# Kernel tuning notes

Hardware: AMD Instinct MI355X
Metric: run time of the kernel (lower is better)

Reference implementation:

```python
import jax, jax.numpy as jnp
from jax import lax
import numpy as np

CLIP = 20.0  # DeepSpeech clipped-ReLU bound


def setup_inputs() -> dict:
    key = jax.random.key(0)
    k1, k2, k3 = jax.random.split(key, 3)
    B, T, F, U_ = 32, 800, 161, 1024
    inputs = jax.random.normal(k1, (B, T, F), dtype=jnp.float32)
    W = jax.random.normal(k2, (F, U_), dtype=jnp.float32) * 0.05
    U = jax.random.normal(k3, (U_, U_), dtype=jnp.float32) * 0.02
    b = jnp.zeros((U_,), dtype=jnp.float32)
    return {"inputs": inputs, "W": W, "U": U, "b": b}


def reference(inputs, W, U, b):
    # inputs: [B, T, F]; shared cell weights for both directions.
    B = inputs.shape[0]
    units = U.shape[0]
    # Precompute input projection for all timesteps: [T, B, units]
    xW = (jnp.einsum('btf,fu->btu', inputs, W) + b).transpose(1, 0, 2)
    h0 = jnp.zeros((B, units), dtype=inputs.dtype)

    def step(h, x):
        h = jnp.minimum(jax.nn.relu(x + h @ U), CLIP)
        return h, None

    hf, _ = lax.scan(step, h0, xW)                 # final state, forward direction
    hb, _ = lax.scan(step, h0, xW, reverse=True)   # final state, go_backwards
    return hf + hb
```

## Files before the change

kernel.cpp:

```cpp
#include <hip/hip_runtime.h>
#include <hip/hip_bf16.h>

#define T_STEPS 800
#define BATCH   32
#define FEAT    161
#define UNITS   1024
#define CLIPV   20.0f

typedef __attribute__((ext_vector_type(8))) short short8;
typedef __attribute__((ext_vector_type(4))) float f32x4;
typedef unsigned short u16;
typedef unsigned int   u32;
typedef unsigned long long u64;

__device__ __forceinline__ float bf16_f(u16 u) {
    return __uint_as_float(((u32)u) << 16);
}
__device__ __forceinline__ u16 bf16_rn(float x) {
    __hip_bfloat16 b = __float2bfloat16(x);
    return *(u16*)&b;
}
__device__ __forceinline__ u64 ld_agent_u64(const u64* p) {
    return __hip_atomic_load(p, __ATOMIC_RELAXED, __HIP_MEMORY_SCOPE_AGENT);
}
__device__ __forceinline__ float ld_agent_f(const float* p) {
    return __hip_atomic_load(p, __ATOMIC_RELAXED, __HIP_MEMORY_SCOPE_AGENT);
}
__device__ __forceinline__ void st_agent_f(float* p, float v) {
    __hip_atomic_store(p, v, __ATOMIC_RELAXED, __HIP_MEMORY_SCOPE_AGENT);
}
__device__ __forceinline__ void st_agent_u32(u32* p, u32 v) {
    __hip_atomic_store(p, v, __ATOMIC_RELAXED, __HIP_MEMORY_SCOPE_AGENT);
}
__device__ __forceinline__ short8 ld_agent_b16x8(const u16* p) {
    union { u64 q[2]; short8 v; } u;
    u.q[0] = ld_agent_u64((const u64*)p);
    u.q[1] = ld_agent_u64((const u64*)p + 1);
    return u.v;
}

__global__ __launch_bounds__(256) void init_ws(float* hbuf, u32* flags) {
    int gid = blockIdx.x * 256 + threadIdx.x;
    for (int i = gid; i < 2 * 64 * UNITS; i += 64 * 256) hbuf[i] = 0.f;
    if (gid < 256) flags[gid] = 0u;
}

__global__ __launch_bounds__(256) void u_split_t(const float* __restrict__ U,
                                                 u16* __restrict__ Ut1,
                                                 u16* __restrict__ Ut2,
                                                 u16* __restrict__ Ut3) {
    __shared__ float tile[32][33];
    int bx = blockIdx.x, by = blockIdx.y;
    int lx = threadIdx.x & 31;
    int ly4 = (threadIdx.x >> 5) * 4;
    #pragma unroll
    for (int j = 0; j < 4; ++j)
        tile[ly4 + j][lx] = U[(size_t)(by * 32 + ly4 + j) * UNITS + bx * 32 + lx];
    __syncthreads();
    #pragma unroll
    for (int j = 0; j < 4; ++j) {
        float x = tile[lx][ly4 + j];
        size_t o = (size_t)(bx * 32 + ly4 + j) * UNITS + by * 32 + lx;
        u16 s1 = bf16_rn(x);  float r1 = x - bf16_f(s1);
        u16 s2 = bf16_rn(r1); float r2 = r1 - bf16_f(s2);
        u16 s3 = bf16_rn(r2);
        Ut1[o] = s1; Ut2[o] = s2; Ut3[o] = s3;
    }
}

__global__ __launch_bounds__(256) void xw_gemm(const float* __restrict__ inp,
                                               const float* __restrict__ W,
                                               const float* __restrict__ bias,
                                               float* __restrict__ xW) {
    __shared__ float xs[8 * FEAT];
    int t = blockIdx.x;
    int b0 = blockIdx.y * 8;
    int tid = threadIdx.x;

    for (int i = tid; i < 8 * FEAT; i += 256) {
        int j = i / FEAT;
        int f = i - j * FEAT;
        xs[i] = inp[((size_t)(b0 + j) * T_STEPS + t) * FEAT + f];
    }
    __syncthreads();

    float bv[4];
    #pragma unroll
    for (int c = 0; c < 4; ++c) bv[c] = bias[tid + c * 256];

    float acc[8][4];
    #pragma unroll
    for (int j = 0; j < 8; ++j)
        #pragma unroll
        for (int c = 0; c < 4; ++c) acc[j][c] = bv[c];

    for (int f = 0; f < FEAT; ++f) {
        float w0 = W[(size_t)f * UNITS + tid];
        float w1 = W[(size_t)f * UNITS + tid + 256];
        float w2 = W[(size_t)f * UNITS + tid + 512];
        float w3 = W[(size_t)f * UNITS + tid + 768];
        #pragma unroll
        for (int j = 0; j < 8; ++j) {
            float xv = xs[j * FEAT + f];
            acc[j][0] += xv * w0;
            acc[j][1] += xv * w1;
            acc[j][2] += xv * w2;
            acc[j][3] += xv * w3;
        }
    }

    #pragma unroll
    for (int j = 0; j < 8; ++j)
        #pragma unroll
        for (int c = 0; c < 4; ++c)
            xW[((size_t)t * BATCH + b0 + j) * UNITS + tid + c * 256] = acc[j][c];
}

__global__ __launch_bounds__(512) void rnn_scan(
        const float* __restrict__ xW,
        const u16* __restrict__ Ut1, const u16* __restrict__ Ut2,
        const u16* __restrict__ Ut3,
        float* __restrict__ hbuf, u32* __restrict__ flags,
        float* __restrict__ out) {
    __shared__ f32x4 red[14][64];

    const int tid  = threadIdx.x;
    const int bk   = blockIdx.x;
    const int lane = tid & 63;
    const int kq   = tid >> 6;
    const int quad = lane >> 4;
    const int n16  = lane & 15;
    const int rg   = bk & 3;
    const int ug   = bk >> 2;
    const int R0   = rg * 16;
    const int u0   = ug * 32;
    const int dir  = rg >> 1;

    short8 bfr[4][2][3];
    #pragma unroll
    for (int ks = 0; ks < 4; ++ks) {
        const int koff = kq * 128 + ks * 32 + quad * 8;
        #pragma unroll
        for (int nq = 0; nq < 2; ++nq) {
            const size_t ub = (size_t)(u0 + nq * 16 + n16) * UNITS + koff;
            bfr[ks][nq][0] = ld_agent_b16x8(Ut1 + ub);
            bfr[ks][nq][1] = ld_agent_b16x8(Ut2 + ub);
            bfr[ks][nq][2] = ld_agent_b16x8(Ut3 + ub);
        }
    }

    const size_t HS = (size_t)64 * UNITS;
    u32* myflag = flags + rg * 32 + ug;
    const u64* srcflag = (const u64*)(flags + rg * 32 + kq * 4);

    for (int t = 0; t < T_STEPS; ++t) {
        const size_t sb = (size_t)(t & 1) * HS;
        const size_t db = sb ^ HS;

        float xp[2][4];
        if (kq == 0) {
            const int xt = dir ? (T_STEPS - 1 - t) : t;
            #pragma unroll
            for (int nq = 0; nq < 2; ++nq)
                #pragma unroll
                for (int j = 0; j < 4; ++j) {
                    const int b = (R0 + quad * 4 + j) & 31;
                    xp[nq][j] = xW[(size_t)xt * (BATCH * UNITS) +
                                   (size_t)b * UNITS + u0 + nq * 16 + n16];
                }
        }

        const u32 tgt = (u32)t;
        for (;;) {
            u64 qa = ld_agent_u64(srcflag);
            u64 qb = ld_agent_u64(srcflag + 1);
            u32 f0 = (u32)qa, f1 = (u32)(qa >> 32);
            u32 f2 = (u32)qb, f3 = (u32)(qb >> 32);
            if (f0 >= tgt && f1 >= tgt && f2 >= tgt && f3 >= tgt) break;
        }

        f32x4 acc[2][2] = {{{0.f,0.f,0.f,0.f},{0.f,0.f,0.f,0.f}},
                           {{0.f,0.f,0.f,0.f},{0.f,0.f,0.f,0.f}}};
        #pragma unroll
        for (int ks = 0; ks < 4; ++ks) {
            const float* ap = hbuf + sb + (size_t)(R0 + n16) * UNITS +
                              kq * 128 + ks * 32 + quad * 8;
            union { u64 q[4]; float f[8]; u32 u[8]; } hv;
            hv.q[0] = ld_agent_u64((const u64*)ap);
            hv.q[1] = ld_agent_u64((const u64*)ap + 1);
            hv.q[2] = ld_agent_u64((const u64*)ap + 2);
            hv.q[3] = ld_agent_u64((const u64*)ap + 3);
            short8 a1, a2, a3;
            #pragma unroll
            for (int j = 0; j < 8; ++j) {
                float x = hv.f[j];
                u16 s1 = (u16)(hv.u[j] >> 16);
                float r1 = x - bf16_f(s1);
                u16 s2 = (u16)(__float_as_uint(r1) >> 16);
                float r2 = r1 - bf16_f(s2);
                u16 s3 = (u16)(__float_as_uint(r2) >> 16);
                a1[j] = (short)s1; a2[j] = (short)s2; a3[j] = (short)s3;
            }
            #pragma unroll
            for (int nq = 0; nq < 2; ++nq) {
                acc[nq][0] = __builtin_amdgcn_mfma_f32_16x16x32_bf16(a1, bfr[ks][nq][0], acc[nq][0], 0, 0, 0);
                acc[nq][1] = __builtin_amdgcn_mfma_f32_16x16x32_bf16(a2, bfr[ks][nq][0], acc[nq][1], 0, 0, 0);
                acc[nq][0] = __builtin_amdgcn_mfma_f32_16x16x32_bf16(a1, bfr[ks][nq][1], acc[nq][0], 0, 0, 0);
                acc[nq][1] = __builtin_amdgcn_mfma_f32_16x16x32_bf16(a2, bfr[ks][nq][1], acc[nq][1], 0, 0, 0);
                acc[nq][0] = __builtin_amdgcn_mfma_f32_16x16x32_bf16(a1, bfr[ks][nq][2], acc[nq][0], 0, 0, 0);
                acc[nq][1] = __builtin_amdgcn_mfma_f32_16x16x32_bf16(a3, bfr[ks][nq][0], acc[nq][1], 0, 0, 0);
            }
        }
        f32x4 c0 = acc[0][0] + acc[0][1];
        f32x4 c1 = acc[1][0] + acc[1][1];

        if (kq) {
            red[(kq - 1) * 2 + 0][lane] = c0;
            red[(kq - 1) * 2 + 1][lane] = c1;
        }
        __syncthreads();
        if (kq == 0) {
            #pragma unroll
            for (int w = 0; w < 7; ++w) {
                c0 += red[w * 2 + 0][lane];
                c1 += red[w * 2 + 1][lane];
            }
            float* hdst = hbuf + db;
            #pragma unroll
            for (int nq = 0; nq < 2; ++nq)
                #pragma unroll
                for (int j = 0; j < 4; ++j) {
                    float a = (nq ? c1[j] : c0[j]) + xp[nq][j];
                    a = fminf(fmaxf(a, 0.f), CLIPV);
                    st_agent_f(hdst + (size_t)(R0 + quad * 4 + j) * UNITS +
                               u0 + nq * 16 + n16, a);
                }
        }
        __syncthreads();
        if (tid == 0) st_agent_u32(myflag, (u32)(t + 1));
    }

    if (rg < 2) {
        const u32* bwd = flags + (rg + 2) * 32 + ug;
        while (__hip_atomic_load(bwd, __ATOMIC_RELAXED,
                                 __HIP_MEMORY_SCOPE_AGENT) < (u32)T_STEPS) {}
        const int r = tid >> 5, c = tid & 31;
        const int b = R0 + r;
        float hf = ld_agent_f(hbuf + (size_t)b * UNITS + u0 + c);
        float hb = ld_agent_f(hbuf + (size_t)(b + 32) * UNITS + u0 + c);
        out[(size_t)b * UNITS + u0 + c] = hf + hb;
    }
}

extern "C" void kernel_launch(void* const* d_in, const int* in_sizes, int n_in,
                              void* d_out, int out_size, void* d_ws, size_t ws_size,
                              hipStream_t stream) {
    const float* inp  = (const float*)d_in[0];
    const float* W    = (const float*)d_in[1];
    const float* U    = (const float*)d_in[2];
    const float* bias = (const float*)d_in[3];
    float* out = (float*)d_out;

    u16*   Ut1 = (u16*)d_ws;
    u16*   Ut2 = Ut1 + (size_t)UNITS * UNITS;
    u16*   Ut3 = Ut2 + (size_t)UNITS * UNITS;
    float* xW  = (float*)(Ut3 + (size_t)UNITS * UNITS);
    float* hbuf = xW + (size_t)T_STEPS * BATCH * UNITS;
    u32*   flags = (u32*)(hbuf + (size_t)2 * 64 * UNITS);

    init_ws<<<64, 256, 0, stream>>>(hbuf, flags);
    u_split_t<<<dim3(32, 32), 256, 0, stream>>>(U, Ut1, Ut2, Ut3);
    xw_gemm<<<dim3(800, 4), 256, 0, stream>>>(inp, W, bias, xW);

    void* args[] = {(void*)&xW, (void*)&Ut1, (void*)&Ut2, (void*)&Ut3,
                    (void*)&hbuf, (void*)&flags, (void*)&out};
    hipLaunchCooperativeKernel((const void*)rnn_scan, dim3(128), dim3(512),
                               args, 0, stream);
}
```

Before: 4.332 ms.

## Replace per-block step flags with tagged hidden-state words for inter-block sync

Each hidden-state element is now stored as a 64-bit word that packs the float value with its timestep tag. Consumers spin directly on the data they need, so the separate flag store and the flag poll round-trip go away. The cross-wave reduction and epilogue are also spread over all 512 threads instead of one wave doing the add, clip and store. The cost is doubled hidden-state traffic, 8-byte loads per element, and polling on data words that may contend with producers' stores.

```diff
diff --git a/kernel.cpp b/kernel.cpp
--- a/kernel.cpp
+++ b/kernel.cpp
@@ -23,26 +23,19 @@
 __device__ __forceinline__ u64 ld_agent_u64(const u64* p) {
     return __hip_atomic_load(p, __ATOMIC_RELAXED, __HIP_MEMORY_SCOPE_AGENT);
 }
-__device__ __forceinline__ float ld_agent_f(const float* p) {
-    return __hip_atomic_load(p, __ATOMIC_RELAXED, __HIP_MEMORY_SCOPE_AGENT);
-}
-__device__ __forceinline__ void st_agent_f(float* p, float v) {
+__device__ __forceinline__ void st_agent_u64(u64* p, u64 v) {
     __hip_atomic_store(p, v, __ATOMIC_RELAXED, __HIP_MEMORY_SCOPE_AGENT);
 }
-__device__ __forceinline__ void st_agent_u32(u32* p, u32 v) {
-    __hip_atomic_store(p, v, __ATOMIC_RELAXED, __HIP_MEMORY_SCOPE_AGENT);
-}
-__device__ __forceinline__ short8 ld_agent_b16x8(const u16* p) {
+__device__ __forceinline__ short8 ld_b16x8(const u16* p) {
     union { u64 q[2]; short8 v; } u;
     u.q[0] = ld_agent_u64((const u64*)p);
     u.q[1] = ld_agent_u64((const u64*)p + 1);
     return u.v;
 }
 
-__global__ __launch_bounds__(256) void init_ws(float* hbuf, u32* flags) {
+__global__ __launch_bounds__(256) void init_ws(u64* htag) {
     int gid = blockIdx.x * 256 + threadIdx.x;
-    for (int i = gid; i < 2 * 64 * UNITS; i += 64 * 256) hbuf[i] = 0.f;
-    if (gid < 256) flags[gid] = 0u;
+    for (int i = gid; i < 2 * 64 * UNITS; i += 64 * 256) htag[i] = 0ull;
 }
 
 __global__ __launch_bounds__(256) void u_split_t(const float* __restrict__ U,
@@ -120,9 +113,8 @@
         const float* __restrict__ xW,
         const u16* __restrict__ Ut1, const u16* __restrict__ Ut2,
         const u16* __restrict__ Ut3,
-        float* __restrict__ hbuf, u32* __restrict__ flags,
-        float* __restrict__ out) {
-    __shared__ f32x4 red[14][64];
+        u64* __restrict__ htag, float* __restrict__ out) {
+    __shared__ f32x4 red[16][64];
 
     const int tid  = threadIdx.x;
     const int bk   = blockIdx.x;
@@ -136,6 +128,14 @@
     const int u0   = ug * 32;
     const int dir  = rg >> 1;
 
+    const int erow = tid >> 5;
+    const int ecol = tid & 31;
+    const int enq  = ecol >> 4;
+    const int el16 = (erow >> 2) * 16 + (ecol & 15);
+    const int ereg = erow & 3;
+    const int eb   = (R0 + erow) & 31;
+    const size_t edst = (size_t)(R0 + erow) * UNITS + u0 + ecol;
+
     short8 bfr[4][2][3];
     #pragma unroll
     for (int ks = 0; ks < 4; ++ks) {
@@ -143,58 +143,44 @@
         #pragma unroll
         for (int nq = 0; nq < 2; ++nq) {
             const size_t ub = (size_t)(u0 + nq * 16 + n16) * UNITS + koff;
-            bfr[ks][nq][0] = ld_agent_b16x8(Ut1 + ub);
-            bfr[ks][nq][1] = ld_agent_b16x8(Ut2 + ub);
-            bfr[ks][nq][2] = ld_agent_b16x8(Ut3 + ub);
+            bfr[ks][nq][0] = ld_b16x8(Ut1 + ub);
+            bfr[ks][nq][1] = ld_b16x8(Ut2 + ub);
+            bfr[ks][nq][2] = ld_b16x8(Ut3 + ub);
         }
     }
 
     const size_t HS = (size_t)64 * UNITS;
-    u32* myflag = flags + rg * 32 + ug;
-    const u64* srcflag = (const u64*)(flags + rg * 32 + kq * 4);
 
     for (int t = 0; t < T_STEPS; ++t) {
         const size_t sb = (size_t)(t & 1) * HS;
         const size_t db = sb ^ HS;
-
-        float xp[2][4];
-        if (kq == 0) {
-            const int xt = dir ? (T_STEPS - 1 - t) : t;
-            #pragma unroll
-            for (int nq = 0; nq < 2; ++nq)
-                #pragma unroll
-                for (int j = 0; j < 4; ++j) {
-                    const int b = (R0 + quad * 4 + j) & 31;
-                    xp[nq][j] = xW[(size_t)xt * (BATCH * UNITS) +
-                                   (size_t)b * UNITS + u0 + nq * 16 + n16];
-                }
-        }
-
-        const u32 tgt = (u32)t;
-        for (;;) {
-            u64 qa = ld_agent_u64(srcflag);
-            u64 qb = ld_agent_u64(srcflag + 1);
-            u32 f0 = (u32)qa, f1 = (u32)(qa >> 32);
-            u32 f2 = (u32)qb, f3 = (u32)(qb >> 32);
-            if (f0 >= tgt && f1 >= tgt && f2 >= tgt && f3 >= tgt) break;
-        }
+        const u32 tagv = (u32)t;
+
+        const int xt = dir ? (T_STEPS - 1 - t) : t;
+        const float xwv = xW[(size_t)xt * (BATCH * UNITS) +
+                             (size_t)eb * UNITS + u0 + ecol];
 
         f32x4 acc[2][2] = {{{0.f,0.f,0.f,0.f},{0.f,0.f,0.f,0.f}},
                            {{0.f,0.f,0.f,0.f},{0.f,0.f,0.f,0.f}}};
         #pragma unroll
         for (int ks = 0; ks < 4; ++ks) {
-            const float* ap = hbuf + sb + (size_t)(R0 + n16) * UNITS +
-                              kq * 128 + ks * 32 + quad * 8;
-            union { u64 q[4]; float f[8]; u32 u[8]; } hv;
-            hv.q[0] = ld_agent_u64((const u64*)ap);
-            hv.q[1] = ld_agent_u64((const u64*)ap + 1);
-            hv.q[2] = ld_agent_u64((const u64*)ap + 2);
-            hv.q[3] = ld_agent_u64((const u64*)ap + 3);
+            const u64* src = htag + sb + (size_t)(R0 + n16) * UNITS +
+                             kq * 128 + ks * 32 + quad * 8;
+            u64 p[8];
+            for (;;) {
+                #pragma unroll
+                for (int j = 0; j < 8; ++j) p[j] = ld_agent_u64(src + j);
+                bool ok = true;
+                #pragma unroll
+                for (int j = 0; j < 8; ++j) ok &= ((u32)(p[j] >> 32) == tagv);
+                if (__all(ok)) break;
+            }
             short8 a1, a2, a3;
             #pragma unroll
             for (int j = 0; j < 8; ++j) {
-                float x = hv.f[j];
-                u16 s1 = (u16)(hv.u[j] >> 16);
+                u32 xb = (u32)p[j];
+                float x = __uint_as_float(xb);
+                u16 s1 = (u16)(xb >> 16);
                 float r1 = x - bf16_f(s1);
                 u16 s2 = (u16)(__float_as_uint(r1) >> 16);
                 float r2 = r1 - bf16_f(s2);
@@ -211,44 +197,28 @@
                 acc[nq][1] = __builtin_amdgcn_mfma_f32_16x16x32_bf16(a3, bfr[ks][nq][0], acc[nq][1], 0, 0, 0);
             }
         }
-        f32x4 c0 = acc[0][0] + acc[0][1];
-        f32x4 c1 = acc[1][0] + acc[1][1];
-
-        if (kq) {
-            red[(kq - 1) * 2 + 0][lane] = c0;
-            red[(kq - 1) * 2 + 1][lane] = c1;
-        }
+
+        red[kq * 2 + 0][lane] = acc[0][0] + acc[0][1];
+        red[kq * 2 + 1][lane] = acc[1][0] + acc[1][1];
         __syncthreads();
-        if (kq == 0) {
-            #pragma unroll
-            for (int w = 0; w < 7; ++w) {
-                c0 += red[w * 2 + 0][lane];
-                c1 += red[w * 2 + 1][lane];
-            }
-            float* hdst = hbuf + db;
-            #pragma unroll
-            for (int nq = 0; nq < 2; ++nq)
-                #pragma unroll
-                for (int j = 0; j < 4; ++j) {
-                    float a = (nq ? c1[j] : c0[j]) + xp[nq][j];
-                    a = fminf(fmaxf(a, 0.f), CLIPV);
-                    st_agent_f(hdst + (size_t)(R0 + quad * 4 + j) * UNITS +
-                               u0 + nq * 16 + n16, a);
-                }
-        }
+
+        float s = 0.f;
+        #pragma unroll
+        for (int w = 0; w < 8; ++w) s += red[w * 2 + enq][el16][ereg];
+        float a = fminf(fmaxf(s + xwv, 0.f), CLIPV);
+        st_agent_u64(htag + db + edst,
+                     ((u64)(u32)(t + 1) << 32) | (u64)__float_as_uint(a));
         __syncthreads();
-        if (tid == 0) st_agent_u32(myflag, (u32)(t + 1));
     }
 
     if (rg < 2) {
-        const u32* bwd = flags + (rg + 2) * 32 + ug;
-        while (__hip_atomic_load(bwd, __ATOMIC_RELAXED,
-                                 __HIP_MEMORY_SCOPE_AGENT) < (u32)T_STEPS) {}
-        const int r = tid >> 5, c = tid & 31;
-        const int b = R0 + r;
-        float hf = ld_agent_f(hbuf + (size_t)b * UNITS + u0 + c);
-        float hb = ld_agent_f(hbuf + (size_t)(b + 32) * UNITS + u0 + c);
-        out[(size_t)b * UNITS + u0 + c] = hf + hb;
+        const u64* pf = htag + (size_t)(R0 + erow) * UNITS + u0 + ecol;
+        const u64* pb = htag + (size_t)(R0 + erow + 32) * UNITS + u0 + ecol;
+        u64 vf, vb;
+        while ((u32)((vf = ld_agent_u64(pf)) >> 32) != (u32)T_STEPS) {}
+        while ((u32)((vb = ld_agent_u64(pb)) >> 32) != (u32)T_STEPS) {}
+        out[(size_t)(R0 + erow) * UNITS + u0 + ecol] =
+            __uint_as_float((u32)vf) + __uint_as_float((u32)vb);
     }
 }
 
@@ -265,15 +235,14 @@
     u16*   Ut2 = Ut1 + (size_t)UNITS * UNITS;
     u16*   Ut3 = Ut2 + (size_t)UNITS * UNITS;
     float* xW  = (float*)(Ut3 + (size_t)UNITS * UNITS);
-    float* hbuf = xW + (size_t)T_STEPS * BATCH * UNITS;
-    u32*   flags = (u32*)(hbuf + (size_t)2 * 64 * UNITS);
-
-    init_ws<<<64, 256, 0, stream>>>(hbuf, flags);
+    u64*   htag = (u64*)(xW + (size_t)T_STEPS * BATCH * UNITS);
+
+    init_ws<<<64, 256, 0, stream>>>(htag);
     u_split_t<<<dim3(32, 32), 256, 0, stream>>>(U, Ut1, Ut2, Ut3);
     xw_gemm<<<dim3(800, 4), 256, 0, stream>>>(inp, W, bias, xW);
 
     void* args[] = {(void*)&xW, (void*)&Ut1, (void*)&Ut2, (void*)&Ut3,
-                    (void*)&hbuf, (void*)&flags, (void*)&out};
+                    (void*)&htag, (void*)&out};
     hipLaunchCooperativeKernel((const void*)rnn_scan, dim3(128), dim3(512),
                                args, 0, stream);
 }
```

New measurement: 7.198 ms. 1.66x slower.

## Pin each row group to one XCD and sync via XCD-local L2 with fallback

Applied to the files above, without the earlier changes.

Launches 256 blocks and keeps only those whose block index maps to XCD groups 0-3, so each batch-row group's 32 blocks are intended to share one XCD. Hidden-state and flag traffic then uses plain stores and sc0 loads that stay in the local L2, avoiding the agent-scope coherence path. A runtime XCD-ID check picks the mode. A poll timeout demotes a group to the agent-scope protocol if the placement assumption fails. The final states are copied to a separate buffer and combined across groups after a global counter. This adds inline-asm memory ordering that is hard to verify and depends on how the hardware assigns blocks to XCDs.

```diff
diff --git a/kernel.cpp b/kernel.cpp
--- a/kernel.cpp
+++ b/kernel.cpp
@@ -6,9 +6,11 @@
 #define FEAT    161
 #define UNITS   1024
 #define CLIPV   20.0f
+#define POLL_TIMEOUT 4096
 
 typedef __attribute__((ext_vector_type(8))) short short8;
 typedef __attribute__((ext_vector_type(4))) float f32x4;
+typedef __attribute__((ext_vector_type(4))) unsigned int u32x4;
 typedef unsigned short u16;
 typedef unsigned int   u32;
 typedef unsigned long long u64;
@@ -23,13 +25,16 @@
 __device__ __forceinline__ u64 ld_agent_u64(const u64* p) {
     return __hip_atomic_load(p, __ATOMIC_RELAXED, __HIP_MEMORY_SCOPE_AGENT);
 }
+__device__ __forceinline__ u32 ld_agent_u32(const u32* p) {
+    return __hip_atomic_load(p, __ATOMIC_RELAXED, __HIP_MEMORY_SCOPE_AGENT);
+}
 __device__ __forceinline__ float ld_agent_f(const float* p) {
     return __hip_atomic_load(p, __ATOMIC_RELAXED, __HIP_MEMORY_SCOPE_AGENT);
 }
+__device__ __forceinline__ void st_agent_u32(u32* p, u32 v) {
+    __hip_atomic_store(p, v, __ATOMIC_RELAXED, __HIP_MEMORY_SCOPE_AGENT);
+}
 __device__ __forceinline__ void st_agent_f(float* p, float v) {
-    __hip_atomic_store(p, v, __ATOMIC_RELAXED, __HIP_MEMORY_SCOPE_AGENT);
-}
-__device__ __forceinline__ void st_agent_u32(u32* p, u32 v) {
     __hip_atomic_store(p, v, __ATOMIC_RELAXED, __HIP_MEMORY_SCOPE_AGENT);
 }
 __device__ __forceinline__ short8 ld_agent_b16x8(const u16* p) {
@@ -38,11 +43,54 @@
     u.q[1] = ld_agent_u64((const u64*)p + 1);
     return u.v;
 }
-
-__global__ __launch_bounds__(256) void init_ws(float* hbuf, u32* flags) {
+__device__ __forceinline__ u32x4 ld_sc0_u32x4(const u32* p) {
+    u32x4 v;
+    asm volatile("global_load_dwordx4 %0, %1, off sc0\n\t"
+                 "s_waitcnt vmcnt(0)"
+                 : "=&v"(v) : "v"(p) : "memory");
+    return v;
+}
+__device__ __forceinline__ float ld_sc0_f(const float* p) {
+    float v;
+    asm volatile("global_load_dword %0, %1, off sc0\n\t"
+                 "s_waitcnt vmcnt(0)"
+                 : "=&v"(v) : "v"(p) : "memory");
+    return v;
+}
+__device__ __forceinline__ void st_plain_u32(u32* p, u32 v) {
+    asm volatile("global_store_dword %0, %1, off" :: "v"(p), "v"(v) : "memory");
+}
+__device__ __forceinline__ void st_plain_f(float* p, float v) {
+    asm volatile("global_store_dword %0, %1, off" :: "v"(p), "v"(v) : "memory");
+}
+struct Q8 { f32x4 a, b, c, d, e, f, g, h; };
+__device__ __forceinline__ Q8 ld_sc0_q8(const float* ab) {
+    Q8 r;
+    asm volatile(
+        "global_load_dwordx4 %0, %8, off sc0\n\t"
+        "global_load_dwordx4 %1, %8, off offset:16 sc0\n\t"
+        "global_load_dwordx4 %2, %8, off offset:128 sc0\n\t"
+        "global_load_dwordx4 %3, %8, off offset:144 sc0\n\t"
+        "global_load_dwordx4 %4, %8, off offset:256 sc0\n\t"
+        "global_load_dwordx4 %5, %8, off offset:272 sc0\n\t"
+        "global_load_dwordx4 %6, %8, off offset:384 sc0\n\t"
+        "global_load_dwordx4 %7, %8, off offset:400 sc0\n\t"
+        "s_waitcnt vmcnt(0)"
+        : "=&v"(r.a), "=&v"(r.b), "=&v"(r.c), "=&v"(r.d),
+          "=&v"(r.e), "=&v"(r.f), "=&v"(r.g), "=&v"(r.h)
+        : "v"(ab) : "memory");
+    return r;
+}
+
+#define C_DEMOTE  0
+#define C_NDONE   16
+#define C_FINDONE 24
+#define C_FLAGS   128
+#define C_LOC     256
+
+__global__ __launch_bounds__(256) void init_ws(u32* ctrl) {
     int gid = blockIdx.x * 256 + threadIdx.x;
-    for (int i = gid; i < 2 * 64 * UNITS; i += 64 * 256) hbuf[i] = 0.f;
-    if (gid < 256) flags[gid] = 0u;
+    if (gid < 512) st_agent_u32(ctrl + gid, 0u);
 }
 
 __global__ __launch_bounds__(256) void u_split_t(const float* __restrict__ U,
@@ -120,21 +168,45 @@
         const float* __restrict__ xW,
         const u16* __restrict__ Ut1, const u16* __restrict__ Ut2,
         const u16* __restrict__ Ut3,
-        float* __restrict__ hbuf, u32* __restrict__ flags,
-        float* __restrict__ out) {
+        float* __restrict__ hbuf, float* __restrict__ finbuf,
+        u32* __restrict__ ctrl, float* __restrict__ out) {
     __shared__ f32x4 red[14][64];
-
-    const int tid  = threadIdx.x;
-    const int bk   = blockIdx.x;
+    __shared__ u32 s_mode, s_dem;
+
+    const int tid = threadIdx.x;
+    const int bk  = blockIdx.x;
+    const int gg  = bk & 7;
+    if (gg >= 4) return;
+    const int g    = gg;
+    const int slot = bk >> 3;
     const int lane = tid & 63;
     const int kq   = tid >> 6;
     const int quad = lane >> 4;
     const int n16  = lane & 15;
-    const int rg   = bk & 3;
-    const int ug   = bk >> 2;
-    const int R0   = rg * 16;
-    const int u0   = ug * 32;
-    const int dir  = rg >> 1;
+    const int R0   = g * 16;
+    const int u0   = slot * 32;
+    const int dir  = g >> 1;
+
+    u32* flags  = ctrl + C_FLAGS;
+    u32* myflag = flags + g * 32 + slot;
+    const u32* fpoll = flags + g * 32 + kq * 4;
+
+    int xcd;
+    asm volatile("s_getreg_b32 %0, hwreg(HW_REG_XCC_ID)" : "=s"(xcd));
+    xcd &= 7;
+    if (tid == 0) {
+        st_agent_u32(ctrl + C_LOC + g * 32 + slot, (xcd == g) ? 1u : 2u);
+        __hip_atomic_fetch_add(ctrl + C_NDONE, 1u, __ATOMIC_RELAXED,
+                               __HIP_MEMORY_SCOPE_AGENT);
+        while (ld_agent_u32(ctrl + C_NDONE) < 128u) __builtin_amdgcn_s_sleep(2);
+        u32 ok = 1;
+        for (int i = 0; i < 32; ++i)
+            if (ld_agent_u32(ctrl + C_LOC + g * 32 + i) != 1u) ok = 0;
+        s_mode = ok ? 0u : 1u;
+        s_dem = 0u;
+    }
+    __syncthreads();
+    bool stick = false;
 
     short8 bfr[4][2][3];
     #pragma unroll
@@ -149,13 +221,28 @@
         }
     }
 
+    {
+        const bool am0 = (s_mode != 0);
+        const int zr = tid >> 5, zc = tid & 31;
+        float* zp = hbuf + (size_t)(R0 + zr) * UNITS + u0 + zc;
+        st_plain_f(zp, 0.f);
+        if (am0) st_agent_f(zp, 0.f);
+    }
+    __syncthreads();
+    if (tid == 0) {
+        st_plain_u32(myflag, 1u);
+        if (s_mode != 0) st_agent_u32(myflag, 1u);
+    }
+
     const size_t HS = (size_t)64 * UNITS;
-    u32* myflag = flags + rg * 32 + ug;
-    const u64* srcflag = (const u64*)(flags + rg * 32 + kq * 4);
 
     for (int t = 0; t < T_STEPS; ++t) {
         const size_t sb = (size_t)(t & 1) * HS;
         const size_t db = sb ^ HS;
+        const u32 tgt = (u32)(t + 1);
+        const bool am = (s_mode != 0);
+
+        if (tid == 0) s_dem = ld_agent_u32(ctrl + C_DEMOTE + g);
 
         float xp[2][4];
         if (kq == 0) {
@@ -170,31 +257,68 @@
                 }
         }
 
-        const u32 tgt = (u32)t;
-        for (;;) {
-            u64 qa = ld_agent_u64(srcflag);
-            u64 qb = ld_agent_u64(srcflag + 1);
-            u32 f0 = (u32)qa, f1 = (u32)(qa >> 32);
-            u32 f2 = (u32)qb, f3 = (u32)(qb >> 32);
-            if (f0 >= tgt && f1 >= tgt && f2 >= tgt && f3 >= tgt) break;
+        bool am_eff = am || stick;
+        if (!am_eff) {
+            int tries = 0;
+            for (;;) {
+                u32x4 f = ld_sc0_u32x4(fpoll);
+                if (f.x >= tgt && f.y >= tgt && f.z >= tgt && f.w >= tgt) break;
+                if (++tries > POLL_TIMEOUT) {
+                    st_agent_u32(ctrl + C_DEMOTE + g, 1u);
+                    #pragma unroll
+                    for (int j = 0; j < 8; ++j) {
+                        int e = lane * 8 + j;
+                        int r = e >> 5, c = e & 31;
+                        float* p = hbuf + sb + (size_t)(R0 + r) * UNITS + u0 + c;
+                        st_agent_f(p, ld_sc0_f(p));
+                    }
+                    __builtin_amdgcn_s_waitcnt(0);
+                    if (lane == 0) st_agent_u32(myflag, tgt);
+                    stick = true; am_eff = true;
+                    break;
+                }
+            }
+        }
+        if (am_eff) {
+            const u64* sf = (const u64*)fpoll;
+            for (;;) {
+                u64 qa = ld_agent_u64(sf), qb = ld_agent_u64(sf + 1);
+                if ((u32)qa >= tgt && (u32)(qa >> 32) >= tgt &&
+                    (u32)qb >= tgt && (u32)(qb >> 32) >= tgt) break;
+                __builtin_amdgcn_s_sleep(1);
+            }
+        }
+
+        union HU { f32x4 v4[2]; u64 q[2]; float f[8]; u32 u[8]; } hu[4];
+        const float* ab = hbuf + sb + (size_t)(R0 + n16) * UNITS + kq * 128 + quad * 8;
+        if (!am_eff) {
+            Q8 q8 = ld_sc0_q8(ab);
+            hu[0].v4[0] = q8.a; hu[0].v4[1] = q8.b;
+            hu[1].v4[0] = q8.c; hu[1].v4[1] = q8.d;
+            hu[2].v4[0] = q8.e; hu[2].v4[1] = q8.f;
+            hu[3].v4[0] = q8.g; hu[3].v4[1] = q8.h;
+        } else {
+            #pragma unroll
+            for (int ks = 0; ks < 4; ++ks) {
+                const u64* sp = (const u64*)(ab + ks * 32);
+                hu[ks].q[0] = ld_agent_u64(sp);
+                hu[ks].q[1] = ld_agent_u64(sp + 1);
+                const u64* sp2 = sp + 2;
+                ((u64*)&hu[ks].v4[1])[0] = ld_agent_u64(sp2);
+                ((u64*)&hu[ks].v4[1])[1] = ld_agent_u64(sp2 + 1);
+            }
         }
 
         f32x4 acc[2][2] = {{{0.f,0.f,0.f,0.f},{0.f,0.f,0.f,0.f}},
                            {{0.f,0.f,0.f,0.f},{0.f,0.f,0.f,0.f}}};
         #pragma unroll
         for (int ks = 0; ks < 4; ++ks) {
-            const float* ap = hbuf + sb + (size_t)(R0 + n16) * UNITS +
-                              kq * 128 + ks * 32 + quad * 8;
-            union { u64 q[4]; float f[8]; u32 u[8]; } hv;
-            hv.q[0] = ld_agent_u64((const u64*)ap);
-            hv.q[1] = ld_agent_u64((const u64*)ap + 1);
-            hv.q[2] = ld_agent_u64((const u64*)ap + 2);
-            hv.q[3] = ld_agent_u64((const u64*)ap + 3);
             short8 a1, a2, a3;
             #pragma unroll
             for (int j = 0; j < 8; ++j) {
-                float x = hv.f[j];
-                u16 s1 = (u16)(hv.u[j] >> 16);
+                u32 xb = hu[ks].u[j];
+                float x = __uint_as_float(xb);
+                u16 s1 = (u16)(xb >> 16);
                 float r1 = x - bf16_f(s1);
                 u16 s2 = (u16)(__float_as_uint(r1) >> 16);
                 float r2 = r1 - bf16_f(s2);
@@ -225,6 +349,17 @@
                 c0 += red[w * 2 + 0][lane];
                 c1 += red[w * 2 + 1][lane];
             }
+            const bool dem = (s_dem != 0);
+            const bool pub_agent = am || stick || dem;
+            if (!am && dem) {
+                #pragma unroll
+                for (int j = 0; j < 8; ++j) {
+                    int e = lane * 8 + j;
+                    int r = e >> 5, c = e & 31;
+                    float* p = hbuf + sb + (size_t)(R0 + r) * UNITS + u0 + c;
+                    st_agent_f(p, ld_sc0_f(p));
+                }
+            }
             float* hdst = hbuf + db;
             #pragma unroll
             for (int nq = 0; nq < 2; ++nq)
@@ -232,22 +367,41 @@
                 for (int j = 0; j < 4; ++j) {
                     float a = (nq ? c1[j] : c0[j]) + xp[nq][j];
                     a = fminf(fmaxf(a, 0.f), CLIPV);
-                    st_agent_f(hdst + (size_t)(R0 + quad * 4 + j) * UNITS +
-                               u0 + nq * 16 + n16, a);
+                    float* dp = hdst + (size_t)(R0 + quad * 4 + j) * UNITS +
+                                u0 + nq * 16 + n16;
+                    st_plain_f(dp, a);
+                    if (pub_agent) st_agent_f(dp, a);
                 }
+            if (lane == 0 && dem) s_mode = 1u;
         }
         __syncthreads();
-        if (tid == 0) st_agent_u32(myflag, (u32)(t + 1));
-    }
-
-    if (rg < 2) {
-        const u32* bwd = flags + (rg + 2) * 32 + ug;
-        while (__hip_atomic_load(bwd, __ATOMIC_RELAXED,
-                                 __HIP_MEMORY_SCOPE_AGENT) < (u32)T_STEPS) {}
+        if (tid == 0) {
+            st_plain_u32(myflag, (u32)(t + 2));
+            if (s_mode != 0 || stick) st_agent_u32(myflag, (u32)(t + 2));
+        }
+    }
+
+    {
+        const bool amf = (s_mode != 0) || stick;
+        const int r = tid >> 5, c = tid & 31;
+        const size_t off = (size_t)(R0 + r) * UNITS + u0 + c;
+        float v = amf ? ld_agent_f(hbuf + off) : ld_sc0_f(hbuf + off);
+        st_agent_f(finbuf + off, v);
+    }
+    __syncthreads();
+    if (tid == 0)
+        __hip_atomic_fetch_add(ctrl + C_FINDONE, 1u, __ATOMIC_RELAXED,
+                               __HIP_MEMORY_SCOPE_AGENT);
+
+    if (g < 2) {
+        if (tid == 0)
+            while (ld_agent_u32(ctrl + C_FINDONE) < 128u)
+                __builtin_amdgcn_s_sleep(1);
+        __syncthreads();
         const int r = tid >> 5, c = tid & 31;
         const int b = R0 + r;
-        float hf = ld_agent_f(hbuf + (size_t)b * UNITS + u0 + c);
-        float hb = ld_agent_f(hbuf + (size_t)(b + 32) * UNITS + u0 + c);
+        float hf = ld_agent_f(finbuf + (size_t)b * UNITS + u0 + c);
+        float hb = ld_agent_f(finbuf + (size_t)(b + 32) * UNITS + u0 + c);
         out[(size_t)b * UNITS + u0 + c] = hf + hb;
     }
 }
@@ -265,15 +419,16 @@
     u16*   Ut2 = Ut1 + (size_t)UNITS * UNITS;
     u16*   Ut3 = Ut2 + (size_t)UNITS * UNITS;
     float* xW  = (float*)(Ut3 + (size_t)UNITS * UNITS);
-    float* hbuf = xW + (size_t)T_STEPS * BATCH * UNITS;
-    u32*   flags = (u32*)(hbuf + (size_t)2 * 64 * UNITS);
-
-    init_ws<<<64, 256, 0, stream>>>(hbuf, flags);
+    float* hbuf   = xW + (size_t)T_STEPS * BATCH * UNITS;
+    float* finbuf = hbuf + (size_t)2 * 64 * UNITS;
+    u32*   ctrl   = (u32*)(finbuf + (size_t)64 * UNITS);
+
+    init_ws<<<2, 256, 0, stream>>>(ctrl);
     u_split_t<<<dim3(32, 32), 256, 0, stream>>>(U, Ut1, Ut2, Ut3);
     xw_gemm<<<dim3(800, 4), 256, 0, stream>>>(inp, W, bias, xW);
 
     void* args[] = {(void*)&xW, (void*)&Ut1, (void*)&Ut2, (void*)&Ut3,
-                    (void*)&hbuf, (void*)&flags, (void*)&out};
-    hipLaunchCooperativeKernel((const void*)rnn_scan, dim3(128), dim3(512),
+                    (void*)&hbuf, (void*)&finbuf, (void*)&ctrl, (void*)&out};
+    hipLaunchCooperativeKernel((const void*)rnn_scan, dim3(256), dim3(512),
                                args, 0, stream);
 }
```

Result: slower. 8.786 ms (+102.8%).
